# Performance work log

Hardware: AMD Instinct MI355X
Metric: run time of the kernel (lower is better)

The kernel has to match this reference:

```python
import jax, jax.numpy as jnp
import numpy as np
import math

N_HEADS = 16

def _layernorm(x, g, b):
    m = x.mean(-1, keepdims=True)
    v = ((x - m) ** 2).mean(-1, keepdims=True)
    return (x - m) * jax.lax.rsqrt(v + 1e-5) * g + b

def _project(x):
    # Poincare ball (c=1) projection: clip last-dim norm to 1 - eps
    max_norm = 1.0 - 1e-5
    n = jnp.linalg.norm(x, axis=-1, keepdims=True)
    return jnp.where(n > max_norm, x * (max_norm / jnp.maximum(n, 1e-12)), x)


def setup_inputs() -> dict:
    key = jax.random.key(0)
    ks = jax.random.split(key, 8)
    B, L, D = 2, 2048, 1024
    w = lambda k, s: jax.random.normal(k, s, jnp.float32) * 0.02
    return dict(
        x=jax.random.normal(ks[0], (B, L, D), jnp.float32),
        wq=w(ks[1], (D, D)), bq=jnp.zeros((D,), jnp.float32),
        wk=w(ks[2], (D, D)), bk=jnp.zeros((D,), jnp.float32),
        wv=w(ks[3], (D, D)), bv=jnp.zeros((D,), jnp.float32),
        wo=w(ks[4], (D, D)), bo=jnp.zeros((D,), jnp.float32),
        g1=jnp.ones((D,), jnp.float32), b1=jnp.zeros((D,), jnp.float32),
        g2=jnp.ones((D,), jnp.float32), b2=jnp.zeros((D,), jnp.float32),
        w1=w(ks[5], (4 * D, D)), bf1=jnp.zeros((4 * D,), jnp.float32),
        w2=w(ks[6], (D, 4 * D)), bf2=jnp.zeros((D,), jnp.float32),
    )


def reference(x, wq, bq, wk, bk, wv, bv, wo, bo, g1, b1, g2, b2, w1, bf1, w2, bf2):
    B, L, D = x.shape
    H = N_HEADS
    hd = D // H
    temp = math.sqrt(hd)

    xn = _layernorm(x, g1, b1)

    def heads(w, b):
        y = xn @ w.T + b                       # [B, L, D]
        return y.reshape(B, L, H, hd).transpose(0, 2, 1, 3)  # [B, H, L, hd]

    q = _project(heads(wq, bq))
    k = _project(heads(wk, bk))
    v = heads(wv, bv)

    # -||q - k||^2 / temp, via ||q||^2 + ||k||^2 - 2 q.k (same math as the
    # explicit broadcast-diff in the torch code, expressed as a GEMM)
    q2 = (q ** 2).sum(-1)[..., :, None]        # [B, H, L, 1]
    k2 = (k ** 2).sum(-1)[..., None, :]        # [B, H, 1, L]
    qk = jnp.einsum('bhld,bhmd->bhlm', q, k)   # [B, H, L, L]
    scores = -(q2 + k2 - 2.0 * qk) / temp
    attn = jax.nn.softmax(scores, axis=-1)     # dropout = identity (eval mode)

    out = jnp.einsum('bhlm,bhmd->bhld', attn, v)
    out = out.transpose(0, 2, 1, 3).reshape(B, L, D) @ wo.T + bo

    x = _project(x + out)
    xn2 = _layernorm(x, g2, b2)
    h = jax.nn.gelu(xn2 @ w1.T + bf1, approximate=False)  # torch nn.GELU = erf
    x = _project(x + (h @ w2.T + bf2))
    return x
```

## Files before the change

### kernel.cpp

```cpp
#include <hip/hip_runtime.h>
#include <math.h>

#define SEQ_L 2048
#define DM    1024
#define NH    16
#define HD    64
#define BL    4096
#define DFF   4096
#define QKV_S 3072

typedef __attribute__((ext_vector_type(8))) short short8;
typedef __attribute__((ext_vector_type(4))) short s16x4;
typedef __attribute__((ext_vector_type(4))) float f32x4;
typedef __attribute__((ext_vector_type(4))) int   i32x4;

#define C_QK  0.36067376022224085f
#define C_K2  0.18033688011112042f

#if __has_builtin(__builtin_amdgcn_exp2f)
#define EXP2(x) __builtin_amdgcn_exp2f(x)
#else
#define EXP2(x) exp2f(x)
#endif

__device__ __forceinline__ short f2bf(float x) {
    unsigned u = __float_as_uint(x);
    u += 0x7fff + ((u >> 16) & 1);
    return (short)(u >> 16);
}
__device__ __forceinline__ float bf2f(short s) {
    return __uint_as_float(((unsigned)(unsigned short)s) << 16);
}
__device__ __forceinline__ int cvt_pk_bf16(float lo, float hi) {
    int r;
    asm("v_cvt_pk_bf16_f32 %0, %1, %2" : "=v"(r) : "v"(lo), "v"(hi));
    return r;
}

__device__ __forceinline__ float gelu_fast(float x) {
    const float xa = fabsf(x);
    const float z = xa * 0.70710678118654752440f;
    const float t = __builtin_amdgcn_rcpf(fmaf(0.3275911f, z, 1.f));
    float P = fmaf(t, 1.061405429f, -1.453152027f);
    P = fmaf(t, P, 1.421413741f);
    P = fmaf(t, P, -0.284496736f);
    P = fmaf(t, P, 0.254829592f);
    P *= t;
    const float e = __expf(-z * z);
    const float erfp = fmaf(-P, e, 1.f);
    return 0.5f * fmaf(xa, erfp, x);
}

__device__ __forceinline__ float block_sum(float v, float* red, int tid) {
#pragma unroll
    for (int m = 32; m; m >>= 1) v += __shfl_xor(v, m);
    if ((tid & 63) == 0) red[tid >> 6] = v;
    __syncthreads();
    v = red[0] + red[1] + red[2] + red[3];
    __syncthreads();
    return v;
}

__global__ __launch_bounds__(256) void cvt6_kernel(
    const float* __restrict__ wq, const float* __restrict__ wk,
    const float* __restrict__ wv, const float* __restrict__ wo,
    const float* __restrict__ w1, const float* __restrict__ w2,
    short* __restrict__ dst) {
    const size_t i = (size_t)blockIdx.x * 256 + threadIdx.x;
    const float* src;
    size_t off;
    if (i < 1048576) {
        const int seg = (int)(i >> 18);
        off = i & 262143;
        src = seg == 0 ? wq : seg == 1 ? wk : seg == 2 ? wv : wo;
    } else if (i < 2097152) { src = w1; off = i - 1048576; }
    else                    { src = w2; off = i - 2097152; }
    const float4 v = ((const float4*)src)[off];
    const s16x4 o = {f2bf(v.x), f2bf(v.y), f2bf(v.z), f2bf(v.w)};
    ((s16x4*)dst)[i] = o;
}

__global__ __launch_bounds__(256) void ln_bf16_kernel(const float* __restrict__ x,
                                                      const float* __restrict__ g,
                                                      const float* __restrict__ b,
                                                      short* __restrict__ out) {
    const int row = blockIdx.x;
    const int tid = threadIdx.x;
    __shared__ float red[4];
    const float4 xv = *(const float4*)(x + (size_t)row * DM + tid * 4);
    float s = xv.x + xv.y + xv.z + xv.w;
    s = block_sum(s, red, tid);
    const float mean = s * (1.f / (float)DM);
    float dx0 = xv.x - mean, dx1 = xv.y - mean, dx2 = xv.z - mean, dx3 = xv.w - mean;
    float ss = dx0 * dx0 + dx1 * dx1 + dx2 * dx2 + dx3 * dx3;
    ss = block_sum(ss, red, tid);
    const float rs = 1.f / sqrtf(ss * (1.f / (float)DM) + 1e-5f);
    const float4 gv = *(const float4*)(g + tid * 4);
    const float4 bv = *(const float4*)(b + tid * 4);
    const s16x4 ob = {f2bf(dx0 * rs * gv.x + bv.x), f2bf(dx1 * rs * gv.y + bv.y),
                      f2bf(dx2 * rs * gv.z + bv.z), f2bf(dx3 * rs * gv.w + bv.w)};
    *(s16x4*)(out + (size_t)row * DM + tid * 4) = ob;
}

__global__ __launch_bounds__(256) void resproj_kernel(const float* __restrict__ a,
                                                      const float* __restrict__ c,
                                                      float* __restrict__ out) {
    const int row = blockIdx.x;
    const int tid = threadIdx.x;
    __shared__ float red[4];
    const float4 av = *(const float4*)(a + (size_t)row * DM + tid * 4);
    const float4 cv = *(const float4*)(c + (size_t)row * DM + tid * 4);
    float4 sv;
    sv.x = av.x + cv.x; sv.y = av.y + cv.y; sv.z = av.z + cv.z; sv.w = av.w + cv.w;
    float ss = sv.x * sv.x + sv.y * sv.y + sv.z * sv.z + sv.w * sv.w;
    ss = block_sum(ss, red, tid);
    const float n = sqrtf(ss);
    const float mx = 1.f - 1e-5f;
    const float scale = (n > mx) ? (mx / fmaxf(n, 1e-12f)) : 1.f;
    sv.x *= scale; sv.y *= scale; sv.z *= scale; sv.w *= scale;
    *(float4*)(out + (size_t)row * DM + tid * 4) = sv;
}

__global__ __launch_bounds__(256) void resproj2_kernel(const float* __restrict__ a,
                                                       const float* __restrict__ c0,
                                                       const float* __restrict__ c1,
                                                       float* __restrict__ out) {
    const int row = blockIdx.x;
    const int tid = threadIdx.x;
    __shared__ float red[4];
    const float4 av = *(const float4*)(a + (size_t)row * DM + tid * 4);
    const float4 cv = *(const float4*)(c0 + (size_t)row * DM + tid * 4);
    const float4 dv = *(const float4*)(c1 + (size_t)row * DM + tid * 4);
    float4 sv;
    sv.x = av.x + cv.x + dv.x; sv.y = av.y + cv.y + dv.y;
    sv.z = av.z + cv.z + dv.z; sv.w = av.w + cv.w + dv.w;
    float ss = sv.x * sv.x + sv.y * sv.y + sv.z * sv.z + sv.w * sv.w;
    ss = block_sum(ss, red, tid);
    const float n = sqrtf(ss);
    const float mx = 1.f - 1e-5f;
    const float scale = (n > mx) ? (mx / fmaxf(n, 1e-12f)) : 1.f;
    sv.x *= scale; sv.y *= scale; sv.z *= scale; sv.w *= scale;
    *(float4*)(out + (size_t)row * DM + tid * 4) = sv;
}

__global__ __launch_bounds__(256) void qk_prep(const short* __restrict__ qkvB,
                                               short* __restrict__ Qb,
                                               short* __restrict__ Kb,
                                               float* __restrict__ k2) {
    const int tid = threadIdx.x, lane = tid & 63;
    const int vec = blockIdx.x * 4 + (tid >> 6);
    const int row = vec >> 4, h = vec & 15;
    const int b = row >> 11, l = row & 2047;
    const size_t dstv = ((size_t)(b * NH + h) * SEQ_L + l) * HD + lane;
    const float mx = 1.f - 1e-5f;
    {
        const float v = bf2f(qkvB[(size_t)row * QKV_S + h * HD + lane]);
        float s = v * v;
#pragma unroll
        for (int m = 32; m; m >>= 1) s += __shfl_xor(s, m);
        const float n = sqrtf(s);
        const float sc = (n > mx) ? (mx / fmaxf(n, 1e-12f)) : 1.f;
        Qb[dstv] = f2bf(v * sc);
    }
    {
        const float v = bf2f(qkvB[(size_t)row * QKV_S + DM + h * HD + lane]);
        float s = v * v;
#pragma unroll
        for (int m = 32; m; m >>= 1) s += __shfl_xor(s, m);
        const float n = sqrtf(s);
        const float sc = (n > mx) ? (mx / fmaxf(n, 1e-12f)) : 1.f;
        Kb[dstv] = f2bf(v * sc);
        if (lane == 0) k2[(size_t)(b * NH + h) * SEQ_L + l] = s * sc * sc * C_K2;
    }
}

__global__ __launch_bounds__(256) void v_prep(const short* __restrict__ qkvB,
                                              short* __restrict__ Vtb) {
    const int blk = blockIdx.x;
    const int bh = blk >> 5, kt = blk & 31;
    const int b = bh >> 4, h = bh & 15;
    __shared__ short T[64 * 72];
    const int tid = threadIdx.x;
    {
        const int key = tid >> 2, ch = (tid & 3) * 16;
        const size_t src = ((size_t)b * SEQ_L + kt * 64 + key) * QKV_S + 2 * DM + h * HD + ch;
        *(short8*)&T[key * 72 + ch]     = *(const short8*)(qkvB + src);
        *(short8*)&T[key * 72 + ch + 8] = *(const short8*)(qkvB + src + 8);
    }
    __syncthreads();
    const int hd = tid >> 2, kc = (tid & 3) * 16;
    short8 o0, o1;
#pragma unroll
    for (int j = 0; j < 8; ++j) {
        o0[j] = T[(kc + j) * 72 + hd];
        o1[j] = T[(kc + 8 + j) * 72 + hd];
    }
    const int c32 = (kc >> 5) * 32;
    const int h4  = ((kc >> 4) & 1) * 4;
    short* dst = Vtb + ((size_t)bh * HD + hd) * SEQ_L + kt * 64 + c32 + h4;
    const s16x4 w0 = {o0[0], o0[1], o0[2], o0[3]};
    const s16x4 w1 = {o0[4], o0[5], o0[6], o0[7]};
    const s16x4 w2 = {o1[0], o1[1], o1[2], o1[3]};
    const s16x4 w3 = {o1[4], o1[5], o1[6], o1[7]};
    *(s16x4*)(dst)      = w0;
    *(s16x4*)(dst + 8)  = w1;
    *(s16x4*)(dst + 16) = w2;
    *(s16x4*)(dst + 24) = w3;
}

template <int BM, int ACT, int OUTBF, int FUSED, int SPLITK>
__global__ __launch_bounds__(256) void gemm_mfma(
    const short* __restrict__ A, const short* __restrict__ Bw,
    const float* __restrict__ bb0, const float* __restrict__ bb1,
    const float* __restrict__ bb2, void* __restrict__ Cout,
    void* __restrict__ Cout2,
    int M, int N, int K) {
    static_assert(BM == 128, "BK=64 staging assumes BM=128");
    constexpr int RT = BM / 32;
    constexpr int LDSR = 72;
    constexpr bool VEPI = (OUTBF != 0) && (BM == 128);
    constexpr int STAGE_SHORTS = (BM + 128) * LDSR;
    static_assert(!VEPI || STAGE_SHORTS >= 4 * 64 * 72, "VEPI smem too small");
    __shared__ __align__(16) short raw[STAGE_SHORTS];
    short* As = raw;
    short* Bs = raw + BM * LDSR;
    const int tid = threadIdx.x;
    const int wv = tid >> 6, lane = tid & 63;

    const int gx = gridDim.x, gy = gridDim.y;
    const int nwg = gx * gy * gridDim.z;
    int d = blockIdx.x + gx * (blockIdx.y + gy * blockIdx.z);
    d = (d & 7) * (nwg >> 3) + (d >> 3);
    const int bx = d % gx;
    const int byz = d / gx;
    const int by = byz % gy;
    const int bz = byz / gy;

    const int m0 = by * BM, n0 = bx * 128;
    const int wr = (wv & 1) * (BM / 2);
    const int wc = (wv >> 1) * 64;

    const int z = (SPLITK > 1) ? bz : 0;
    const int Kc = K / SPLITK;

    const int srow = tid >> 3, sc8 = (tid & 7) * 8;
    const short* Ag = A + (size_t)(m0 + srow) * K + z * Kc + sc8;
    const short* Bg = Bw + (size_t)(n0 + srow) * K + z * Kc + sc8;
    short* AsW = As + srow * LDSR + sc8;
    short* BsW = Bs + srow * LDSR + sc8;

    const f32x4 z4 = {0.f, 0.f, 0.f, 0.f};
    f32x4 acc[RT][4];
#pragma unroll
    for (int r = 0; r < RT; ++r)
#pragma unroll
        for (int c = 0; c < 4; ++c) acc[r][c] = z4;

    const int lrow = lane & 15, kq = (lane >> 4) * 8;

    short8 ra[4], rb[4];
#pragma unroll
    for (int j = 0; j < 4; ++j) {
        ra[j] = *(const short8*)(Ag + (size_t)(32 * j) * K);
        rb[j] = *(const short8*)(Bg + (size_t)(32 * j) * K);
    }

    for (int kt = 0; kt < Kc; kt += 64) {
        __syncthreads();
#pragma unroll
        for (int j = 0; j < 4; ++j) {
            *(short8*)(AsW + (32 * j) * LDSR) = ra[j];
            *(short8*)(BsW + (32 * j) * LDSR) = rb[j];
        }
        if (kt + 64 < Kc) {
#pragma unroll
            for (int j = 0; j < 4; ++j) {
                ra[j] = *(const short8*)(Ag + (size_t)(32 * j) * K + kt + 64);
                rb[j] = *(const short8*)(Bg + (size_t)(32 * j) * K + kt + 64);
            }
        }
        __syncthreads();
#pragma unroll
        for (int h = 0; h < 2; ++h) {
            short8 af[RT], bf[4];
#pragma unroll
            for (int r = 0; r < RT; ++r)
                af[r] = *(const short8*)&As[(wr + r * 16 + lrow) * LDSR + h * 32 + kq];
#pragma unroll
            for (int c = 0; c < 4; ++c)
                bf[c] = *(const short8*)&Bs[(wc + c * 16 + lrow) * LDSR + h * 32 + kq];
#pragma unroll
            for (int r = 0; r < RT; ++r)
#pragma unroll
                for (int c = 0; c < 4; ++c)
                    acc[r][c] = __builtin_amdgcn_mfma_f32_16x16x32_bf16(af[r], bf[c], acc[r][c], 0, 0, 0);
        }
    }

    void* Cbase = Cout;
    if constexpr (SPLITK > 1) { if (z) Cbase = Cout2; }

    const int col = lane & 15, rb4 = (lane >> 4) * 4;
    if constexpr (VEPI) {
        __syncthreads();
        short* Ot = raw + wv * (64 * 72);
#pragma unroll
        for (int c = 0; c < 4; ++c) {
            const int gn = n0 + wc + c * 16 + col;
            float bias;
            if constexpr (FUSED) {
                const int seg = gn >> 10;
                bias = (seg == 0 ? bb0 : seg == 1 ? bb1 : bb2)[gn & 1023];
            } else {
                bias = bb0[gn];
            }
#pragma unroll
            for (int r = 0; r < RT; ++r)
#pragma unroll
                for (int i = 0; i < 4; ++i) {
                    float v = acc[r][c][i] + bias;
                    if constexpr (ACT) v = gelu_fast(v);
                    Ot[(r * 16 + rb4 + i) * 72 + c * 16 + col] = f2bf(v);
                }
        }
        const int orow = lane >> 3, oc = (lane & 7) * 8;
#pragma unroll
        for (int it = 0; it < 8; ++it) {
            const short8 vv = *(const short8*)&Ot[(it * 8 + orow) * 72 + oc];
            *(short8*)((short*)Cbase + (size_t)(m0 + wr + it * 8 + orow) * N + n0 + wc + oc) = vv;
        }
    } else {
#pragma unroll
        for (int c = 0; c < 4; ++c) {
            const int gn = n0 + wc + c * 16 + col;
            float bias;
            if constexpr (FUSED) {
                const int seg = gn >> 10;
                bias = (seg == 0 ? bb0 : seg == 1 ? bb1 : bb2)[gn & 1023];
            } else {
                bias = bb0[gn];
            }
            if constexpr (SPLITK > 1) { if (z) bias = 0.f; }
#pragma unroll
            for (int r = 0; r < RT; ++r) {
                const int gm = m0 + wr + r * 16 + rb4;
#pragma unroll
                for (int i = 0; i < 4; ++i) {
                    float v = acc[r][c][i] + bias;
                    if constexpr (ACT) v = gelu_fast(v);
                    if constexpr (OUTBF)
                        ((short*)Cbase)[(size_t)(gm + i) * N + gn] = f2bf(v);
                    else
                        ((float*)Cbase)[(size_t)(gm + i) * N + gn] = v;
                }
            }
        }
    }
}

__global__ __launch_bounds__(256) void attn_mfma2(const short* __restrict__ Qb,
                                                  const short* __restrict__ Kb,
                                                  const short* __restrict__ Vtb,
                                                  const float* __restrict__ k2v,
                                                  short* __restrict__ aO) {
    int d = blockIdx.x + 16 * (blockIdx.y + 16 * blockIdx.z);
    d = (d & 7) * 64 + (d >> 3);
    const int qt = d & 15, h = (d >> 4) & 15, b = d >> 8;
    const int tid = threadIdx.x, wv = tid >> 6, lane = tid & 63;
    const int bh = b * NH + h;
    constexpr int NT = SEQ_L / 64;
    constexpr int BUFS = 64 * 72;
    __shared__ __align__(16) short smem[4 * BUFS];
    __shared__ __align__(16) float k2s[SEQ_L];
    const int lrow = lane & 15, q8 = (lane >> 4) * 8, q4 = (lane >> 4) * 4;

    const short* Qh = Qb + (size_t)bh * SEQ_L * HD;
    const short* Kh = Kb + (size_t)bh * SEQ_L * HD;
    const short* Vh = Vtb + (size_t)bh * HD * SEQ_L;
    const float* k2p = k2v + (size_t)bh * SEQ_L;

    short8 qf[2][2];
#pragma unroll
    for (int nt = 0; nt < 2; ++nt)
#pragma unroll
        for (int kc = 0; kc < 2; ++kc)
            qf[nt][kc] = *(const short8*)(Qh +
                (size_t)(qt * 128 + wv * 32 + nt * 16 + lrow) * HD + kc * 32 + q8);

    {
        const float4 a0 = *(const float4*)(k2p + tid * 4);
        const float4 a1 = *(const float4*)(k2p + 1024 + tid * 4);
        *(float4*)&k2s[tid * 4] = a0;
        *(float4*)&k2s[1024 + tid * 4] = a1;
    }

    const int srow = tid >> 2, sch = (tid & 3) * 16;
    const short* gK = Kh + (size_t)srow * HD + sch;
    const short* gV = Vh + (size_t)srow * SEQ_L + sch;
    const int woff = srow * 72 + sch;

    {
        const short8 k0a = *(const short8*)(gK);
        const short8 k0b = *(const short8*)(gK + 8);
        const short8 v0a = *(const short8*)(gV);
        const short8 v0b = *(const short8*)(gV + 8);
        *(short8*)&smem[woff]            = k0a;
        *(short8*)&smem[woff + 8]        = k0b;
        *(short8*)&smem[BUFS + woff]     = v0a;
        *(short8*)&smem[BUFS + woff + 8] = v0b;
    }
    __syncthreads();

    const f32x4 z4 = {0.f, 0.f, 0.f, 0.f};
    f32x4 o[4][2];
#pragma unroll
    for (int ht = 0; ht < 4; ++ht)
#pragma unroll
        for (int nt = 0; nt < 2; ++nt) o[ht][nt] = z4;
    float lsum[2] = {0.f, 0.f};

    for (int kt = 0; kt < NT; ++kt) {
        const int k0 = kt * 64;
        const short* Ks = smem + (kt & 1) * (2 * BUFS);
        const short* Vt = Ks + BUFS;
        short8 nk0, nk1, nv0, nv1;
        const bool more = (kt + 1 < NT);
        if (more) {
            const short* g = gK + (size_t)(k0 + 64) * HD;
            nk0 = *(const short8*)(g);
            nk1 = *(const short8*)(g + 8);
            const short* gv2 = gV + (k0 + 64);
            nv0 = *(const short8*)(gv2);
            nv1 = *(const short8*)(gv2 + 8);
        }

        i32x4 pw[2][2];
#pragma unroll
        for (int mt = 0; mt < 4; ++mt) {
            const short8 kf0 = *(const short8*)&Ks[(mt * 16 + lrow) * 72 + q8];
            const short8 kf1 = *(const short8*)&Ks[(mt * 16 + lrow) * 72 + 32 + q8];
            const float4 kk = *(const float4*)&k2s[k0 + mt * 16 + q4];
            const int c = mt >> 1, wb = (mt & 1) * 2;
#pragma unroll
            for (int nt = 0; nt < 2; ++nt) {
                f32x4 s = z4;
                s = __builtin_amdgcn_mfma_f32_16x16x32_bf16(kf0, qf[nt][0], s, 0, 0, 0);
                s = __builtin_amdgcn_mfma_f32_16x16x32_bf16(kf1, qf[nt][1], s, 0, 0, 0);
                const float p0 = EXP2(fmaf(s[0], C_QK, -kk.x));
                const float p1 = EXP2(fmaf(s[1], C_QK, -kk.y));
                const float p2 = EXP2(fmaf(s[2], C_QK, -kk.z));
                const float p3 = EXP2(fmaf(s[3], C_QK, -kk.w));
                lsum[nt] += (p0 + p1) + (p2 + p3);
                pw[nt][c][wb]     = cvt_pk_bf16(p0, p1);
                pw[nt][c][wb + 1] = cvt_pk_bf16(p2, p3);
            }
        }
#pragma unroll
        for (int ht = 0; ht < 4; ++ht) {
#pragma unroll
            for (int c = 0; c < 2; ++c) {
                const short8 v8 = *(const short8*)&Vt[(ht * 16 + lrow) * 72 + c * 32 + q4 * 2];
#pragma unroll
                for (int nt = 0; nt < 2; ++nt)
                    o[ht][nt] = __builtin_amdgcn_mfma_f32_16x16x32_bf16(
                        v8, __builtin_bit_cast(short8, pw[nt][c]), o[ht][nt], 0, 0, 0);
            }
        }

        if (more) {
            short* Kd = smem + ((kt + 1) & 1) * (2 * BUFS);
            *(short8*)&Kd[woff]            = nk0;
            *(short8*)&Kd[woff + 8]        = nk1;
            *(short8*)&Kd[BUFS + woff]     = nv0;
            *(short8*)&Kd[BUFS + woff + 8] = nv1;
        }
        __syncthreads();
    }

#pragma unroll
    for (int nt = 0; nt < 2; ++nt) {
        lsum[nt] += __shfl_xor(lsum[nt], 16);
        lsum[nt] += __shfl_xor(lsum[nt], 32);
    }
    const float inv0 = 1.f / lsum[0], inv1 = 1.f / lsum[1];

    short* Ot = smem + wv * (32 * 72);
#pragma unroll
    for (int ht = 0; ht < 4; ++ht)
#pragma unroll
        for (int nt = 0; nt < 2; ++nt) {
            const float iv = nt ? inv1 : inv0;
            const s16x4 ov = {f2bf(o[ht][nt][0] * iv), f2bf(o[ht][nt][1] * iv),
                              f2bf(o[ht][nt][2] * iv), f2bf(o[ht][nt][3] * iv)};
            *(s16x4*)&Ot[(nt * 16 + lrow) * 72 + ht * 16 + q4] = ov;
        }
    const int erow = lane >> 1, ec = (lane & 1) * 32;
    const short8 r0 = *(const short8*)&Ot[erow * 72 + ec + 0];
    const short8 r1 = *(const short8*)&Ot[erow * 72 + ec + 8];
    const short8 r2 = *(const short8*)&Ot[erow * 72 + ec + 16];
    const short8 r3 = *(const short8*)&Ot[erow * 72 + ec + 24];
    short* dst = aO + ((size_t)b * SEQ_L + qt * 128 + wv * 32 + erow) * DM + h * HD + ec;
    *(short8*)(dst + 0)  = r0;
    *(short8*)(dst + 8)  = r1;
    *(short8*)(dst + 16) = r2;
    *(short8*)(dst + 24) = r3;
}

extern "C" void kernel_launch(void* const* d_in, const int* in_sizes, int n_in,
                              void* d_out, int out_size, void* d_ws, size_t ws_size,
                              hipStream_t stream) {
    const float* x   = (const float*)d_in[0];
    const float* wq  = (const float*)d_in[1];
    const float* bq  = (const float*)d_in[2];
    const float* wk  = (const float*)d_in[3];
    const float* bk  = (const float*)d_in[4];
    const float* wv  = (const float*)d_in[5];
    const float* bv  = (const float*)d_in[6];
    const float* wo  = (const float*)d_in[7];
    const float* bo  = (const float*)d_in[8];
    const float* g1  = (const float*)d_in[9];
    const float* b1  = (const float*)d_in[10];
    const float* g2  = (const float*)d_in[11];
    const float* b2  = (const float*)d_in[12];
    const float* w1  = (const float*)d_in[13];
    const float* bf1 = (const float*)d_in[14];
    const float* w2  = (const float*)d_in[15];
    const float* bf2 = (const float*)d_in[16];
    float* out = (float*)d_out;

    char* base = (char*)d_ws;
    short* wbf  = (short*)base;
    short* qkvB = (short*)(base + (24u << 20));
    short* xnb  = (short*)(base + (48u << 20));
    short* Qb   = xnb;
    short* Kb   = (short*)(base + (56u << 20));
    short* Vtb  = (short*)(base + (64u << 20));
    float* k2   = (float*)(base + (72u << 20));
    short* aO   = (short*)(base + (72u << 20) + (256u << 10));
    float* P    = (float*)(base + (24u << 20));
    float* P2   = (float*)(base + (40u << 20));
    short* xn2b = Vtb;
    short* hbuf = qkvB;
    float* y0   = (float*)base;
    float* y1   = (float*)(base + (56u << 20));

    cvt6_kernel<<<12288, 256, 0, stream>>>(wq, wk, wv, wo, w1, w2, wbf);
    ln_bf16_kernel<<<BL, 256, 0, stream>>>(x, g1, b1, xnb);
    gemm_mfma<128, 0, 1, 1, 1><<<dim3(24, 32), 256, 0, stream>>>(
        xnb, wbf, bq, bk, bv, qkvB, nullptr, BL, QKV_S, DM);
    qk_prep<<<16384, 256, 0, stream>>>(qkvB, Qb, Kb, k2);
    v_prep<<<1024, 256, 0, stream>>>(qkvB, Vtb);
    attn_mfma2<<<dim3(16, 16, 2), 256, 0, stream>>>(Qb, Kb, Vtb, k2, aO);
    gemm_mfma<128, 0, 0, 0, 2><<<dim3(8, 32, 2), 256, 0, stream>>>(
        aO, wbf + 3145728, bo, bo, bo, P, P2, BL, DM, DM);
    resproj2_kernel<<<BL, 256, 0, stream>>>(x, P, P2, out);
    ln_bf16_kernel<<<BL, 256, 0, stream>>>(out, g2, b2, xn2b);
    gemm_mfma<128, 1, 1, 0, 1><<<dim3(32, 32), 256, 0, stream>>>(
        xn2b, wbf + 4194304, bf1, bf1, bf1, hbuf, nullptr, BL, DFF, DM);
    gemm_mfma<128, 0, 0, 0, 2><<<dim3(8, 32, 2), 256, 0, stream>>>(
        hbuf, wbf + 8388608, bf2, bf2, bf2, y0, y1, BL, DM, DFF);
    resproj2_kernel<<<BL, 256, 0, stream>>>(out, y0, y1, out);
}
```

Baseline: 378.8 us.

## Stage GEMM tiles via direct global-to-LDS loads with XOR swizzle; fuse residual+LN

The MFMA GEMM now copies A and B tiles straight from global memory into LDS with 16-byte global_load_lds, replacing the register-staged copy. It switches from a padded 72-wide LDS row to an unpadded 64-wide row with an XOR-swizzled column layout to avoid bank conflicts, which also shrinks shared memory. This drops the register prefetch of the next K-tile, so global loads and MFMA no longer overlap within a workgroup and it relies on occupancy instead. Separately, the post-attention residual projection and the second LayerNorm are merged into one kernel, saving one launch and one global read of the residual.

```diff
diff --git a/kernel.cpp b/kernel.cpp
--- a/kernel.cpp
+++ b/kernel.cpp
@@ -35,6 +35,11 @@
     int r;
     asm("v_cvt_pk_bf16_f32 %0, %1, %2" : "=v"(r) : "v"(lo), "v"(hi));
     return r;
+}
+__device__ __forceinline__ void async_copy16(const short* gsrc, short* ldst) {
+    __builtin_amdgcn_global_load_lds(
+        (const __attribute__((address_space(1))) unsigned int*)gsrc,
+        (__attribute__((address_space(3))) unsigned int*)ldst, 16, 0, 0);
 }
 
 __device__ __forceinline__ float gelu_fast(float x) {
@@ -102,25 +107,6 @@
     *(s16x4*)(out + (size_t)row * DM + tid * 4) = ob;
 }
 
-__global__ __launch_bounds__(256) void resproj_kernel(const float* __restrict__ a,
-                                                      const float* __restrict__ c,
-                                                      float* __restrict__ out) {
-    const int row = blockIdx.x;
-    const int tid = threadIdx.x;
-    __shared__ float red[4];
-    const float4 av = *(const float4*)(a + (size_t)row * DM + tid * 4);
-    const float4 cv = *(const float4*)(c + (size_t)row * DM + tid * 4);
-    float4 sv;
-    sv.x = av.x + cv.x; sv.y = av.y + cv.y; sv.z = av.z + cv.z; sv.w = av.w + cv.w;
-    float ss = sv.x * sv.x + sv.y * sv.y + sv.z * sv.z + sv.w * sv.w;
-    ss = block_sum(ss, red, tid);
-    const float n = sqrtf(ss);
-    const float mx = 1.f - 1e-5f;
-    const float scale = (n > mx) ? (mx / fmaxf(n, 1e-12f)) : 1.f;
-    sv.x *= scale; sv.y *= scale; sv.z *= scale; sv.w *= scale;
-    *(float4*)(out + (size_t)row * DM + tid * 4) = sv;
-}
-
 __global__ __launch_bounds__(256) void resproj2_kernel(const float* __restrict__ a,
                                                        const float* __restrict__ c0,
                                                        const float* __restrict__ c1,
@@ -143,6 +129,42 @@
     *(float4*)(out + (size_t)row * DM + tid * 4) = sv;
 }
 
+__global__ __launch_bounds__(256) void resproj2_ln_kernel(
+    const float* __restrict__ a, const float* __restrict__ c0,
+    const float* __restrict__ c1, const float* __restrict__ g,
+    const float* __restrict__ b, float* __restrict__ out,
+    short* __restrict__ obf) {
+    const int row = blockIdx.x;
+    const int tid = threadIdx.x;
+    __shared__ float red[4];
+    const float4 av = *(const float4*)(a + (size_t)row * DM + tid * 4);
+    const float4 cv = *(const float4*)(c0 + (size_t)row * DM + tid * 4);
+    const float4 dv = *(const float4*)(c1 + (size_t)row * DM + tid * 4);
+    float4 sv;
+    sv.x = av.x + cv.x + dv.x; sv.y = av.y + cv.y + dv.y;
+    sv.z = av.z + cv.z + dv.z; sv.w = av.w + cv.w + dv.w;
+    float ss = sv.x * sv.x + sv.y * sv.y + sv.z * sv.z + sv.w * sv.w;
+    ss = block_sum(ss, red, tid);
+    const float n = sqrtf(ss);
+    const float mx = 1.f - 1e-5f;
+    const float scale = (n > mx) ? (mx / fmaxf(n, 1e-12f)) : 1.f;
+    sv.x *= scale; sv.y *= scale; sv.z *= scale; sv.w *= scale;
+    *(float4*)(out + (size_t)row * DM + tid * 4) = sv;
+    float s = sv.x + sv.y + sv.z + sv.w;
+    s = block_sum(s, red, tid);
+    const float mean = s * (1.f / (float)DM);
+    const float dx0 = sv.x - mean, dx1 = sv.y - mean,
+                dx2 = sv.z - mean, dx3 = sv.w - mean;
+    float s2 = dx0 * dx0 + dx1 * dx1 + dx2 * dx2 + dx3 * dx3;
+    s2 = block_sum(s2, red, tid);
+    const float rs = 1.f / sqrtf(s2 * (1.f / (float)DM) + 1e-5f);
+    const float4 gv = *(const float4*)(g + tid * 4);
+    const float4 bv = *(const float4*)(b + tid * 4);
+    const s16x4 ob = {f2bf(dx0 * rs * gv.x + bv.x), f2bf(dx1 * rs * gv.y + bv.y),
+                      f2bf(dx2 * rs * gv.z + bv.z), f2bf(dx3 * rs * gv.w + bv.w)};
+    *(s16x4*)(obf + (size_t)row * DM + tid * 4) = ob;
+}
+
 __global__ __launch_bounds__(256) void qk_prep(const short* __restrict__ qkvB,
                                                short* __restrict__ Qb,
                                                short* __restrict__ Kb,
@@ -215,15 +237,13 @@
     const float* __restrict__ bb2, void* __restrict__ Cout,
     void* __restrict__ Cout2,
     int M, int N, int K) {
-    static_assert(BM == 128, "BK=64 staging assumes BM=128");
+    static_assert(BM == 128, "staging assumes BM=128");
     constexpr int RT = BM / 32;
-    constexpr int LDSR = 72;
     constexpr bool VEPI = (OUTBF != 0) && (BM == 128);
-    constexpr int STAGE_SHORTS = (BM + 128) * LDSR;
-    static_assert(!VEPI || STAGE_SHORTS >= 4 * 64 * 72, "VEPI smem too small");
-    __shared__ __align__(16) short raw[STAGE_SHORTS];
+    constexpr int RAWS = VEPI ? (4 * 64 * 72) : (2 * 128 * 64);
+    __shared__ __align__(16) short raw[RAWS];
     short* As = raw;
-    short* Bs = raw + BM * LDSR;
+    short* Bs = raw + 128 * 64;
     const int tid = threadIdx.x;
     const int wv = tid >> 6, lane = tid & 63;
 
@@ -243,11 +263,12 @@
     const int z = (SPLITK > 1) ? bz : 0;
     const int Kc = K / SPLITK;
 
-    const int srow = tid >> 3, sc8 = (tid & 7) * 8;
-    const short* Ag = A + (size_t)(m0 + srow) * K + z * Kc + sc8;
-    const short* Bg = Bw + (size_t)(n0 + srow) * K + z * Kc + sc8;
-    short* AsW = As + srow * LDSR + sc8;
-    short* BsW = Bs + srow * LDSR + sc8;
+    const int srl = lane >> 3;
+    const int scol = ((lane & 7) ^ srl) * 8;
+    const short* Ag = A + (size_t)(m0 + wv * 32 + srl) * K + z * Kc + scol;
+    const short* Bg = Bw + (size_t)(n0 + wv * 32 + srl) * K + z * Kc + scol;
+    short* AsW = As + (wv * 32) * 64;
+    short* BsW = Bs + (wv * 32) * 64;
 
     const f32x4 z4 = {0.f, 0.f, 0.f, 0.f};
     f32x4 acc[RT][4];
@@ -256,39 +277,28 @@
 #pragma unroll
         for (int c = 0; c < 4; ++c) acc[r][c] = z4;
 
-    const int lrow = lane & 15, kq = (lane >> 4) * 8;
-
-    short8 ra[4], rb[4];
-#pragma unroll
-    for (int j = 0; j < 4; ++j) {
-        ra[j] = *(const short8*)(Ag + (size_t)(32 * j) * K);
-        rb[j] = *(const short8*)(Bg + (size_t)(32 * j) * K);
-    }
+    const int lrow = lane & 15;
+    const int roff0 = (((lane >> 4)) ^ (lane & 7)) * 8;
+    const int roff1 = ((4 + (lane >> 4)) ^ (lane & 7)) * 8;
 
     for (int kt = 0; kt < Kc; kt += 64) {
         __syncthreads();
 #pragma unroll
         for (int j = 0; j < 4; ++j) {
-            *(short8*)(AsW + (32 * j) * LDSR) = ra[j];
-            *(short8*)(BsW + (32 * j) * LDSR) = rb[j];
-        }
-        if (kt + 64 < Kc) {
-#pragma unroll
-            for (int j = 0; j < 4; ++j) {
-                ra[j] = *(const short8*)(Ag + (size_t)(32 * j) * K + kt + 64);
-                rb[j] = *(const short8*)(Bg + (size_t)(32 * j) * K + kt + 64);
-            }
+            async_copy16(Ag + (size_t)(j * 8) * K + kt, AsW + j * 512);
+            async_copy16(Bg + (size_t)(j * 8) * K + kt, BsW + j * 512);
         }
         __syncthreads();
 #pragma unroll
         for (int h = 0; h < 2; ++h) {
+            const int ro = h ? roff1 : roff0;
             short8 af[RT], bf[4];
 #pragma unroll
             for (int r = 0; r < RT; ++r)
-                af[r] = *(const short8*)&As[(wr + r * 16 + lrow) * LDSR + h * 32 + kq];
+                af[r] = *(const short8*)&As[(wr + r * 16 + lrow) * 64 + ro];
 #pragma unroll
             for (int c = 0; c < 4; ++c)
-                bf[c] = *(const short8*)&Bs[(wc + c * 16 + lrow) * LDSR + h * 32 + kq];
+                bf[c] = *(const short8*)&Bs[(wc + c * 16 + lrow) * 64 + ro];
 #pragma unroll
             for (int r = 0; r < RT; ++r)
 #pragma unroll
@@ -553,8 +563,7 @@
     attn_mfma2<<<dim3(16, 16, 2), 256, 0, stream>>>(Qb, Kb, Vtb, k2, aO);
     gemm_mfma<128, 0, 0, 0, 2><<<dim3(8, 32, 2), 256, 0, stream>>>(
         aO, wbf + 3145728, bo, bo, bo, P, P2, BL, DM, DM);
-    resproj2_kernel<<<BL, 256, 0, stream>>>(x, P, P2, out);
-    ln_bf16_kernel<<<BL, 256, 0, stream>>>(out, g2, b2, xn2b);
+    resproj2_ln_kernel<<<BL, 256, 0, stream>>>(x, P, P2, g2, b2, out, xn2b);
     gemm_mfma<128, 1, 1, 0, 1><<<dim3(32, 32), 256, 0, stream>>>(
         xn2b, wbf + 4194304, bf1, bf1, bf1, hbuf, nullptr, BL, DFF, DM);
     gemm_mfma<128, 0, 0, 0, 2><<<dim3(8, 32, 2), 256, 0, stream>>>(
```

Result: no change. 378.8 us (-0.0%).
